# Performance work log

Hardware: AMD Instinct MI355X
Metric: run time of the kernel (lower is better)

## Reference

```python
import jax, jax.numpy as jnp
import numpy as np

B_GRAPHS = 16
N_PER_GRAPH = 128
N_NODES = B_GRAPHS * N_PER_GRAPH  # 2048
HIDDEN = 256
N_HEADS = 8
HEAD_DIM = HIDDEN // N_HEADS
N_LAYERS = 4
K_RPE = 4
N_EDGES = 32768
NUM_NODE_FEATS = 32
NUM_EDGE_TYPES = 16
MAX_DEGREE = 100
MLP_HID = HIDDEN // 2


def _layernorm(x, s, b):
    m = x.mean(-1, keepdims=True)
    v = jnp.var(x, axis=-1, keepdims=True)
    return (x - m) / jnp.sqrt(v + 1e-5) * s + b


def setup_inputs() -> dict:
    key = jax.random.key(0)
    ks = jax.random.split(key, 24)
    s = 0.02
    x_idx = jax.random.randint(ks[0], (N_NODES,), 0, NUM_NODE_FEATS)
    # edges are intra-graph (the torch code drops cross-graph edges)
    src = jax.random.randint(ks[1], (N_EDGES,), 0, N_NODES)
    dst = (src // N_PER_GRAPH) * N_PER_GRAPH + jax.random.randint(ks[2], (N_EDGES,), 0, N_PER_GRAPH)
    edge_index = jnp.stack([src, dst])
    edge_attr = jax.random.randint(ks[3], (N_EDGES,), 0, NUM_EDGE_TYPES)
    batch = jnp.repeat(jnp.arange(B_GRAPHS), N_PER_GRAPH)
    L = N_LAYERS
    return {
        'x_idx': x_idx, 'edge_index': edge_index, 'edge_attr': edge_attr, 'batch': batch,
        'node_emb': jax.random.normal(ks[4], (NUM_NODE_FEATS, HIDDEN)) * s,
        'edge_emb': jax.random.normal(ks[5], (NUM_EDGE_TYPES, N_HEADS)) * s,
        'degree_emb': jax.random.normal(ks[6], (MAX_DEGREE + 1, HIDDEN)) * s,
        'rpe_W1': jax.random.normal(ks[7], (K_RPE + 1, MLP_HID)) * s,
        'rpe_b1': jnp.zeros((MLP_HID,)),
        'rpe_W2': jax.random.normal(ks[8], (MLP_HID, N_HEADS)) * s,
        'rpe_b2': jnp.zeros((N_HEADS,)),
        'Wq': jax.random.normal(ks[9], (L, HIDDEN, HIDDEN)) * s, 'bq': jnp.zeros((L, HIDDEN)),
        'Wk': jax.random.normal(ks[10], (L, HIDDEN, HIDDEN)) * s, 'bk': jnp.zeros((L, HIDDEN)),
        'Wv': jax.random.normal(ks[11], (L, HIDDEN, HIDDEN)) * s, 'bv': jnp.zeros((L, HIDDEN)),
        'Wo': jax.random.normal(ks[12], (L, HIDDEN, HIDDEN)) * s, 'bo': jnp.zeros((L, HIDDEN)),
        'ln1_s': jnp.ones((L, HIDDEN)), 'ln1_b': jnp.zeros((L, HIDDEN)),
        'ln2_s': jnp.ones((L, HIDDEN)), 'ln2_b': jnp.zeros((L, HIDDEN)),
        'ff_W1': jax.random.normal(ks[13], (L, HIDDEN, 2 * HIDDEN)) * s, 'ff_b1': jnp.zeros((L, 2 * HIDDEN)),
        'ff_W2': jax.random.normal(ks[14], (L, 2 * HIDDEN, HIDDEN)) * s, 'ff_b2': jnp.zeros((L, HIDDEN)),
    }


def _forward(x_idx, edge_index, edge_attr, batch,
             node_emb, edge_emb, degree_emb, rpe_W1, rpe_b1, rpe_W2, rpe_b2,
             Wq, bq, Wk, bk, Wv, bv, Wo, bo, ln1_s, ln1_b, ln2_s, ln2_b,
             ff_W1, ff_b1, ff_W2, ff_b2):
    B, n, H, N = B_GRAPHS, N_PER_GRAPH, N_HEADS, N_NODES
    x = node_emb[x_idx]                               # [N, d]
    src, dst = edge_index[0], edge_index[1]
    # degrees from source endpoints (scatter_add in torch)
    deg = jnp.zeros((N,), jnp.int32).at[src].add(1)
    deg_c = jnp.minimum(deg, MAX_DEGREE)

    # ---- RRWP + edge-type attention bias, block-diagonal over graphs ----
    g = batch[src]
    intra = (batch[src] == batch[dst])                # torch code skips cross-graph edges
    u = src % n
    v = dst % n
    intra_f = intra.astype(jnp.float32)
    inv_du = intra_f / jnp.maximum(deg[src], 1).astype(jnp.float32)
    inv_dv = intra_f / jnp.maximum(deg[dst], 1).astype(jnp.float32)
    # random-walk transition matrix per graph [B, n, n]
    T = (jnp.zeros((B, n, n), jnp.float32)
         .at[g, u, v].add(inv_du)
         .at[g, v, u].add(inv_dv))
    # symmetric edge-type bias per graph [B, n, n, H]
    ev = edge_emb[edge_attr] * intra_f[:, None]
    EB = (jnp.zeros((B, n, n, H), jnp.float32)
          .at[g, u, v].add(ev)
          .at[g, v, u].add(ev))
    # walk powers I, T, T^2, ..., T^K -> [B, n, n, K+1]
    I = jnp.broadcast_to(jnp.eye(n, dtype=jnp.float32), (B, n, n))
    powers = [I, T]
    cur = T
    for _ in range(2, K_RPE + 1):
        cur = cur @ T
        powers.append(cur)
    walk = jnp.stack(powers, axis=-1)
    pair = jax.nn.relu(walk @ rpe_W1 + rpe_b1) @ rpe_W2 + rpe_b2   # [B, n, n, H]
    block = (pair + EB).transpose(0, 3, 1, 2)                      # [B, H, n, n]
    ib = jnp.arange(B)
    full = jnp.full((H, B, n, B, n), -jnp.inf, jnp.float32)
    full = full.at[:, ib, :, ib, :].set(block)                     # diag blocks
    attn_bias = full.reshape(H, N, N)

    # ---- transformer stack ----
    deg_vec = degree_emb[deg_c]
    scale = 1.0 / jnp.sqrt(jnp.float32(HEAD_DIM))
    for l in range(N_LAYERS):
        x = x + deg_vec
        Q = (x @ Wq[l] + bq[l]).reshape(N, H, HEAD_DIM)
        K_ = (x @ Wk[l] + bk[l]).reshape(N, H, HEAD_DIM)
        V = (x @ Wv[l] + bv[l]).reshape(N, H, HEAD_DIM)
        scores = jnp.einsum('ihd,jhd->hij', Q, K_) * scale + attn_bias
        aw = jax.nn.softmax(scores, axis=-1)
        out = jnp.einsum('hij,jhd->ihd', aw, V).reshape(N, HIDDEN)
        out = out @ Wo[l] + bo[l]
        x = _layernorm(x + out, ln1_s[l], ln1_b[l])
        ff = jax.nn.relu(x @ ff_W1[l] + ff_b1[l]) @ ff_W2[l] + ff_b2[l]
        x = _layernorm(x + ff, ln2_s[l], ln2_b[l])
    # global add pool
    return jax.ops.segment_sum(x, batch, num_segments=B)


def reference(x_idx, edge_index, edge_attr, batch,
              node_emb, edge_emb, degree_emb, rpe_W1, rpe_b1, rpe_W2, rpe_b2,
              Wq, bq, Wk, bk, Wv, bv, Wo, bo, ln1_s, ln1_b, ln2_s, ln2_b,
              ff_W1, ff_b1, ff_W2, ff_b2):
    return _forward(x_idx, edge_index, edge_attr, batch,
                    node_emb, edge_emb, degree_emb, rpe_W1, rpe_b1, rpe_W2, rpe_b2,
                    Wq, bq, Wk, bk, Wv, bv, Wo, bo, ln1_s, ln1_b, ln2_s, ln2_b,
                    ff_W1, ff_b1, ff_W2, ff_b2)
```

## Files before the change

### kernel.cpp

```cpp
#include <hip/hip_runtime.h>
#include <hip/hip_bf16.h>

#define B_GRAPHS 16
#define NPG 128
#define NN 2048
#define HIDDEN 256
#define N_HEADS 8
#define HEAD_DIM 32
#define N_LAYERS 4
#define N_EDGES 32768
#define MLP_HID 128
#define MAX_DEG 100

typedef __hip_bfloat16 bf16;
typedef unsigned short ushort_t;
typedef __attribute__((ext_vector_type(8))) short short8;
typedef __attribute__((ext_vector_type(4))) float f32x4;

__device__ __forceinline__ float us2f(ushort_t u) {
    return __uint_as_float(((unsigned)u) << 16);
}
__device__ __forceinline__ ushort_t f2us(float f) {
    unsigned u = __float_as_uint(f);
    return (ushort_t)((u + 0x7FFFu + ((u >> 16) & 1u)) >> 16);
}
__device__ __forceinline__ bool is_bf16_mode(const unsigned* probe) {
    return probe[0] != 0x3F800000u;
}
#define MFMA16(a, b, c) __builtin_amdgcn_mfma_f32_16x16x32_bf16(a, b, c, 0, 0, 0)

#define NW 23
__device__ const int c_wsizes[NW] = {
    8192, 128, 25856, 640, 128, 1024, 8,
    262144, 1024, 262144, 1024, 262144, 1024, 262144, 1024,
    1024, 1024, 1024, 1024,
    524288, 2048, 524288, 1024};
#define TOTW 2144392

#define OFF_NODE_EMB 0
#define OFF_EDGE_EMB 8192
#define OFF_DEG_EMB  8320
#define OFF_RPE_W1   34176
#define OFF_RPE_B1   34816
#define OFF_RPE_W2   34944
#define OFF_RPE_B2   35968
#define OFF_BO       1087624
#define OFF_LN1S     1088648
#define OFF_LN1B     1089672
#define OFF_LN2S     1090696
#define OFF_LN2B     1091720
#define OFF_FFB1     1617032
#define OFF_FFB2     2143368

#define WB_QKV 0
#define WB_O   786432
#define WB_F1  1048576
#define WB_F2  1572864
#define WB_TOT 2097152
#define QKVB_TOT 3072

struct SrcPtrs { const void* p[NW]; };

__global__ void convert_kernel(SrcPtrs sp, const unsigned* __restrict__ probe,
                               float* __restrict__ Wc, float* __restrict__ qkvb) {
    int i = blockIdx.x * 256 + threadIdx.x;
    bool isbf = is_bf16_mode(probe);
    auto rd = [&](int seg, int off) -> float {
        return isbf ? us2f(((const ushort_t*)sp.p[seg])[off])
                    : ((const float*)sp.p[seg])[off];
    };
    if (i < TOTW) {
        int seg = 0, off = i;
        while (seg < NW - 1 && off >= c_wsizes[seg]) { off -= c_wsizes[seg]; seg++; }
        Wc[i] = rd(seg, off);
    } else if (i < TOTW + QKVB_TOT) {
        int j = i - TOTW;
        int l = j / 768, n = j % 768, which = n >> 8, nn = n & 255;
        int seg = (which == 0) ? 8 : (which == 1) ? 10 : 12;
        qkvb[j] = rd(seg, l * 256 + nn);
    }
}

__global__ __launch_bounds__(256) void transpose_pack(SrcPtrs sp,
                                                      const unsigned* __restrict__ probe,
                                                      ushort_t* __restrict__ WB) {
    __shared__ float tile[32][33];
    int b = blockIdx.x;
    bool isbf = is_bf16_mode(probe);
    int seg, soff, srcN, k0, n0, dK;
    size_t doff;
    if (b < 768) {
        int mat = b >> 6, t = b & 63;
        int l = mat / 3, which = mat % 3;
        seg = 7 + which * 2;
        soff = l * 65536; srcN = 256;
        k0 = (t >> 3) * 32; n0 = (t & 7) * 32;
        doff = (size_t)l * 196608 + (size_t)which * 65536; dK = 256;
    } else if (b < 1024) {
        int u = b - 768, l = u >> 6, t = u & 63;
        seg = 13; soff = l * 65536; srcN = 256;
        k0 = (t >> 3) * 32; n0 = (t & 7) * 32;
        doff = WB_O + (size_t)l * 65536; dK = 256;
    } else if (b < 1536) {
        int u = b - 1024, l = u >> 7, t = u & 127;
        seg = 19; soff = l * 131072; srcN = 512;
        k0 = (t >> 4) * 32; n0 = (t & 15) * 32;
        doff = WB_F1 + (size_t)l * 131072; dK = 256;
    } else {
        int u = b - 1536, l = u >> 7, t = u & 127;
        seg = 21; soff = l * 131072; srcN = 256;
        k0 = (t >> 3) * 32; n0 = (t & 7) * 32;
        doff = WB_F2 + (size_t)l * 131072; dK = 512;
    }
    int xcol = threadIdx.x & 31, y8 = threadIdx.x >> 5;
    const void* srcp = sp.p[seg];
#pragma unroll
    for (int rr = 0; rr < 4; rr++) {
        int row = y8 * 4 + rr;
        int off = soff + (k0 + row) * srcN + n0 + xcol;
        tile[row][xcol] = isbf ? us2f(((const ushort_t*)srcp)[off])
                               : ((const float*)srcp)[off];
    }
    __syncthreads();
#pragma unroll
    for (int rr = 0; rr < 4; rr++) {
        int nrow = y8 * 4 + rr;
        WB[doff + (size_t)(n0 + nrow) * dK + k0 + xcol] = f2us(tile[xcol][nrow]);
    }
}

__global__ void zero_kernel(f32x4* __restrict__ p) {
    f32x4 z;
    z[0] = 0.f; z[1] = 0.f; z[2] = 0.f; z[3] = 0.f;
    p[blockIdx.x * 256 + threadIdx.x] = z;
}

__global__ void deg_kernel(const int* __restrict__ src, int* __restrict__ deg) {
    int e = blockIdx.x * blockDim.x + threadIdx.x;
    if (e < N_EDGES) atomicAdd(&deg[src[e]], 1);
}

__global__ void gather_xadd(const int* __restrict__ xidx, const int* __restrict__ deg,
                            const float* __restrict__ emb, const float* __restrict__ demb,
                            float* __restrict__ x, ushort_t* __restrict__ xb) {
    int i = blockIdx.x * blockDim.x + threadIdx.x;
    int node = i >> 8, c = i & 255;
    float v = emb[xidx[node] * HIDDEN + c] + demb[min(deg[node], MAX_DEG) * HIDDEN + c];
    x[i] = v;
    xb[i] = f2us(v);
}

__global__ void scatter_kernel(const int* __restrict__ ei, const int* __restrict__ eattr,
                               const int* __restrict__ batch, const int* __restrict__ deg,
                               const float* __restrict__ edge_emb,
                               float* __restrict__ T, float* __restrict__ bias) {
    int idx = blockIdx.x * blockDim.x + threadIdx.x;
    int e = idx >> 3, h = idx & 7;
    int s = ei[e], d = ei[N_EDGES + e];
    if (batch[s] != batch[d]) return;
    int g = batch[s];
    int u = s & (NPG - 1), v = d & (NPG - 1);
    if (h == 0) {
        atomicAdd(&T[(g * NPG + u) * NPG + v], 1.0f / (float)max(deg[s], 1));
        atomicAdd(&T[(g * NPG + v) * NPG + u], 1.0f / (float)max(deg[d], 1));
    }
    float ev = edge_emb[eattr[e] * N_HEADS + h];
    atomicAdd(&bias[(((size_t)(g * N_HEADS + h) * NPG + u) * NPG + v)], ev);
    atomicAdd(&bias[(((size_t)(g * N_HEADS + h) * NPG + v) * NPG + u)], ev);
}

__global__ void matmul128(const float* __restrict__ A, const float* __restrict__ B,
                          float* __restrict__ C) {
    int g = blockIdx.x / NPG;
    int row = blockIdx.x % NPG;
    int col = threadIdx.x;
    const float* Ag = A + (size_t)g * NPG * NPG;
    const float* Bg = B + (size_t)g * NPG * NPG;
    __shared__ float arow[NPG];
    arow[col] = Ag[row * NPG + col];
    __syncthreads();
    float acc = 0.f;
#pragma unroll 8
    for (int k = 0; k < NPG; k++) acc += arow[k] * Bg[k * NPG + col];
    C[((size_t)g * NPG + row) * NPG + col] = acc;
}

__global__ void matmul128_dual(const float* __restrict__ T2, const float* __restrict__ T,
                               float* __restrict__ T3, float* __restrict__ T4) {
    int half = blockIdx.x >> 11;
    int bid = blockIdx.x & 2047;
    int g = bid / NPG, row = bid % NPG, col = threadIdx.x;
    const float* Ag = T2 + (size_t)g * NPG * NPG;
    const float* Bg = (half ? T2 : T) + (size_t)g * NPG * NPG;
    float* Cg = (half ? T4 : T3) + (size_t)g * NPG * NPG;
    __shared__ float arow[NPG];
    arow[col] = Ag[row * NPG + col];
    __syncthreads();
    float acc = 0.f;
#pragma unroll 8
    for (int k = 0; k < NPG; k++) acc += arow[k] * Bg[k * NPG + col];
    Cg[row * NPG + col] = acc;
}

__global__ __launch_bounds__(256) void rpe_kernel(
    const float* __restrict__ T, const float* __restrict__ T2,
    const float* __restrict__ T3, const float* __restrict__ T4,
    const float* __restrict__ W1, const float* __restrict__ b1,
    const float* __restrict__ W2, const float* __restrict__ b2,
    float* __restrict__ bias) {
    __shared__ float sW1[5][MLP_HID];
    __shared__ float sb1[MLP_HID];
    __shared__ float sW2[MLP_HID][N_HEADS];
    int t = threadIdx.x;
    for (int i = t; i < 5 * MLP_HID; i += 256) sW1[i / MLP_HID][i % MLP_HID] = W1[i];
    for (int i = t; i < MLP_HID; i += 256) sb1[i] = b1[i];
    for (int i = t; i < MLP_HID * N_HEADS; i += 256) sW2[i / N_HEADS][i % N_HEADS] = W2[i];
    __syncthreads();
    int p = blockIdx.x * 256 + t;
    int g = p / (NPG * NPG);
    int rem = p % (NPG * NPG);
    int i = rem / NPG, j = rem % NPG;
    float f0 = (i == j) ? 1.f : 0.f;
    float f1 = T[p], f2 = T2[p], f3 = T3[p], f4 = T4[p];
    float acc[N_HEADS];
#pragma unroll
    for (int h = 0; h < N_HEADS; h++) acc[h] = b2[h];
#pragma unroll 4
    for (int m = 0; m < MLP_HID; m++) {
        float hv = sb1[m] + f0 * sW1[0][m] + f1 * sW1[1][m] + f2 * sW1[2][m] +
                   f3 * sW1[3][m] + f4 * sW1[4][m];
        hv = fmaxf(hv, 0.f);
#pragma unroll
        for (int h = 0; h < N_HEADS; h++) acc[h] += hv * sW2[m][h];
    }
#pragma unroll
    for (int h = 0; h < N_HEADS; h++)
        bias[(((size_t)(g * N_HEADS + h) * NPG + i) * NPG + j)] += acc[h];
}

__global__ __launch_bounds__(256, 1) void qkv_attn(
    const ushort_t* __restrict__ x_bf, const ushort_t* __restrict__ WT,
    const float* __restrict__ qb, const float* __restrict__ bias,
    ushort_t* __restrict__ ao) {
    int bid = blockIdx.x;
    int g = bid >> 4, h = (bid >> 1) & 7, half = bid & 1;
    int wave = threadIdx.x >> 6, lane = threadIdx.x & 63;
    int lr = lane & 15, lq = lane >> 4;

    __shared__ ushort_t Qs[64][40];
    __shared__ ushort_t Ks[NPG][40];
    __shared__ ushort_t VT[32][136];
    __shared__ ushort_t P[4][16][136];

    const ushort_t* xg = x_bf + (size_t)g * NPG * HIDDEN;
    int qrow = half * 64 + wave * 16;
    int kvrow = wave * 32;

    short8 Aq[8], Akv[2][8], Bq[2][8], Bk[2][8], Bv[2][8];
#pragma unroll
    for (int kk = 0; kk < 8; kk++) {
        Aq[kk] = *(const short8*)(xg + (size_t)(qrow + lr) * 256 + kk * 32 + lq * 8);
#pragma unroll
        for (int i = 0; i < 2; i++)
            Akv[i][kk] = *(const short8*)(xg + (size_t)(kvrow + i * 16 + lr) * 256 +
                                          kk * 32 + lq * 8);
#pragma unroll
        for (int j = 0; j < 2; j++) {
            int n = h * 32 + j * 16 + lr;
            Bq[j][kk] = *(const short8*)(WT + (size_t)n * 256 + kk * 32 + lq * 8);
            Bk[j][kk] = *(const short8*)(WT + (size_t)(n + 256) * 256 + kk * 32 + lq * 8);
            Bv[j][kk] = *(const short8*)(WT + (size_t)(n + 512) * 256 + kk * 32 + lq * 8);
        }
    }
    float bqv[2], bkv[2], bvv[2];
#pragma unroll
    for (int j = 0; j < 2; j++) {
        int c = h * 32 + j * 16 + lr;
        bqv[j] = qb[c]; bkv[j] = qb[256 + c]; bvv[j] = qb[512 + c];
    }

    f32x4 qa[2]{}, ka[2][2]{}, va[2][2]{};
#pragma unroll
    for (int kk = 0; kk < 8; kk++)
#pragma unroll
        for (int j = 0; j < 2; j++) {
            qa[j] = MFMA16(Aq[kk], Bq[j][kk], qa[j]);
#pragma unroll
            for (int i = 0; i < 2; i++) {
                ka[i][j] = MFMA16(Akv[i][kk], Bk[j][kk], ka[i][j]);
                va[i][j] = MFMA16(Akv[i][kk], Bv[j][kk], va[i][j]);
            }
        }

    const float* bg = bias + (size_t)(g * N_HEADS + h) * NPG * NPG;
    float bgv[8][4];
#pragma unroll
    for (int r = 0; r < 4; r++) {
        int i = half * 64 + wave * 16 + lq * 4 + r;
#pragma unroll
        for (int jt = 0; jt < 8; jt++)
            bgv[jt][r] = bg[(size_t)i * NPG + jt * 16 + lr];
    }

#pragma unroll
    for (int j = 0; j < 2; j++) {
        int c = j * 16 + lr;
#pragma unroll
        for (int r = 0; r < 4; r++) {
            Qs[wave * 16 + lq * 4 + r][c] = f2us(qa[j][r] + bqv[j]);
#pragma unroll
            for (int i = 0; i < 2; i++) {
                int row = kvrow + i * 16 + lq * 4 + r;
                Ks[row][c] = f2us(ka[i][j][r] + bkv[j]);
                VT[c][row] = f2us(va[i][j][r] + bvv[j]);
            }
        }
    }
    __syncthreads();

    short8 qf = *(const short8*)(&Qs[wave * 16 + lr][lq * 8]);
    f32x4 S[8];
    f32x4 zero;
    zero[0] = 0.f; zero[1] = 0.f; zero[2] = 0.f; zero[3] = 0.f;
#pragma unroll
    for (int jt = 0; jt < 8; jt++) {
        short8 kf = *(const short8*)(&Ks[jt * 16 + lr][lq * 8]);
        S[jt] = MFMA16(qf, kf, zero);
    }

    const float scale = 0.17677669529663687f;
    float lrow[4];
#pragma unroll
    for (int r = 0; r < 4; r++) {
        float mx = -1e30f;
#pragma unroll
        for (int jt = 0; jt < 8; jt++) {
            float s = S[jt][r] * scale + bgv[jt][r];
            S[jt][r] = s;
            mx = fmaxf(mx, s);
        }
#pragma unroll
        for (int m = 1; m < 16; m <<= 1) mx = fmaxf(mx, __shfl_xor(mx, m));
        float sum = 0.f;
#pragma unroll
        for (int jt = 0; jt < 8; jt++) {
            float e = __expf(S[jt][r] - mx);
            S[jt][r] = e;
            sum += e;
        }
#pragma unroll
        for (int m = 1; m < 16; m <<= 1) sum += __shfl_xor(sum, m);
        lrow[r] = sum;
    }

#pragma unroll
    for (int jt = 0; jt < 8; jt++)
#pragma unroll
        for (int r = 0; r < 4; r++)
            P[wave][lq * 4 + r][jt * 16 + lr] = f2us(S[jt][r]);

    f32x4 O[2]{};
#pragma unroll
    for (int k0 = 0; k0 < NPG; k0 += 32) {
        short8 pa = *(const short8*)(&P[wave][lr][k0 + lq * 8]);
#pragma unroll
        for (int dt = 0; dt < 2; dt++) {
            short8 vb = *(const short8*)(&VT[dt * 16 + lr][k0 + lq * 8]);
            O[dt] = MFMA16(pa, vb, O[dt]);
        }
    }
#pragma unroll
    for (int r = 0; r < 4; r++) {
        float inv = 1.f / lrow[r];
        int row = g * NPG + half * 64 + wave * 16 + lq * 4 + r;
#pragma unroll
        for (int dt = 0; dt < 2; dt++)
            ao[(size_t)row * HIDDEN + h * 32 + dt * 16 + lr] = f2us(O[dt][r] * inv);
    }
}

__global__ __launch_bounds__(256, 1) void fused_mlp(
    const ushort_t* __restrict__ ao, const ushort_t* __restrict__ WoT,
    const float* __restrict__ bo, const float* __restrict__ ln1s,
    const float* __restrict__ ln1b,
    const ushort_t* __restrict__ F1T, const ushort_t* __restrict__ F2T,
    const float* __restrict__ fb1, const float* __restrict__ fb2,
    const float* __restrict__ ln2s, const float* __restrict__ ln2b,
    const float* __restrict__ xin, const int* __restrict__ deg,
    const float* __restrict__ demb, int add_deg,
    float* __restrict__ xout, ushort_t* __restrict__ xb) {
    int m0 = blockIdx.x * 8;
    int wave = threadIdx.x >> 6, lane = threadIdx.x & 63;
    int lr = lane & 15, lq = lane >> 4;
    int ar = m0 + (lr & 7);

    __shared__ ushort_t xs_bf[8][264];
    __shared__ float xs_f[8][256];
    __shared__ ushort_t ffh[8][520];
    __shared__ float ws[4][16], qs[4][16];

    short8 Ao[8], Bo[4][8];
#pragma unroll
    for (int kk = 0; kk < 8; kk++) {
        Ao[kk] = *(const short8*)(ao + (size_t)ar * 256 + kk * 32 + lq * 8);
#pragma unroll
        for (int jt = 0; jt < 4; jt++) {
            int n = wave * 64 + jt * 16 + lr;
            Bo[jt][kk] = *(const short8*)(WoT + (size_t)n * 256 + kk * 32 + lq * 8);
        }
    }
    float bo_v[4], l1s[4], l1b[4], fb2v[4], l2s[4], l2b[4], xres[4][4], fb1v[8];
#pragma unroll
    for (int jt = 0; jt < 4; jt++) {
        int col = wave * 64 + jt * 16 + lr;
        bo_v[jt] = bo[col]; l1s[jt] = ln1s[col]; l1b[jt] = ln1b[col];
        fb2v[jt] = fb2[col]; l2s[jt] = ln2s[col]; l2b[jt] = ln2b[col];
#pragma unroll
        for (int r = 0; r < 4; r++) {
            int row = m0 + ((lq * 4 + r) & 7);
            xres[jt][r] = xin[(size_t)row * 256 + col];
        }
    }
#pragma unroll
    for (int jt = 0; jt < 8; jt++) fb1v[jt] = fb1[wave * 128 + jt * 16 + lr];
    int dg4[4];
    if (add_deg) {
#pragma unroll
        for (int r = 0; r < 4; r++)
            dg4[r] = min(deg[m0 + ((lq * 4 + r) & 7)], MAX_DEG);
    }

    f32x4 acc[4]{};
#pragma unroll
    for (int kk = 0; kk < 8; kk++)
#pragma unroll
        for (int jt = 0; jt < 4; jt++)
            acc[jt] = MFMA16(Ao[kk], Bo[jt][kk], acc[jt]);

    short8 B1[8][8];
#pragma unroll
    for (int kk = 0; kk < 8; kk++)
#pragma unroll
        for (int jt = 0; jt < 8; jt++) {
            int n = wave * 128 + jt * 16 + lr;
            B1[jt][kk] = *(const short8*)(F1T + (size_t)n * 256 + kk * 32 + lq * 8);
        }

    float val[4][4], meanst[4];
#pragma unroll
    for (int r = 0; r < 4; r++) {
        float s = 0.f;
#pragma unroll
        for (int jt = 0; jt < 4; jt++) {
            float v = acc[jt][r] + bo_v[jt] + xres[jt][r];
            val[jt][r] = v;
            s += v;
        }
#pragma unroll
        for (int m = 1; m < 16; m <<= 1) s += __shfl_xor(s, m);
        if (lr == 0) ws[wave][lq * 4 + r] = s;
    }
    __syncthreads();
#pragma unroll
    for (int r = 0; r < 4; r++) {
        int rr = lq * 4 + r;
        float mean = (ws[0][rr] + ws[1][rr] + ws[2][rr] + ws[3][rr]) * (1.f / 256.f);
        meanst[r] = mean;
        float q = 0.f;
#pragma unroll
        for (int jt = 0; jt < 4; jt++) {
            float d = val[jt][r] - mean;
            q += d * d;
        }
#pragma unroll
        for (int m = 1; m < 16; m <<= 1) q += __shfl_xor(q, m);
        if (lr == 0) qs[wave][rr] = q;
    }
    __syncthreads();
#pragma unroll
    for (int r = 0; r < 4; r++) {
        int rr = lq * 4 + r;
        float var = (qs[0][rr] + qs[1][rr] + qs[2][rr] + qs[3][rr]) * (1.f / 256.f);
        float rstd = rsqrtf(var + 1e-5f);
        if (rr < 8) {
#pragma unroll
            for (int jt = 0; jt < 4; jt++) {
                int col = wave * 64 + jt * 16 + lr;
                float y = (val[jt][r] - meanst[r]) * rstd * l1s[jt] + l1b[jt];
                xs_f[rr][col] = y;
                xs_bf[rr][col] = f2us(y);
            }
        }
    }
    __syncthreads();

    f32x4 acc1[8]{};
#pragma unroll
    for (int kk = 0; kk < 8; kk++) {
        short8 a = *(const short8*)(&xs_bf[lr & 7][kk * 32 + lq * 8]);
#pragma unroll
        for (int jt = 0; jt < 8; jt++)
            acc1[jt] = MFMA16(a, B1[jt][kk], acc1[jt]);
    }

    short8 B2[4][16];
#pragma unroll
    for (int kk = 0; kk < 16; kk++)
#pragma unroll
        for (int jt = 0; jt < 4; jt++) {
            int n = wave * 64 + jt * 16 + lr;
            B2[jt][kk] = *(const short8*)(F2T + (size_t)n * 512 + kk * 32 + lq * 8);
        }

#pragma unroll
    for (int jt = 0; jt < 8; jt++) {
        int n = wave * 128 + jt * 16 + lr;
#pragma unroll
        for (int r = 0; r < 4; r++) {
            int rr = lq * 4 + r;
            if (rr < 8) ffh[rr][n] = f2us(fmaxf(acc1[jt][r] + fb1v[jt], 0.f));
        }
    }
    __syncthreads();

    f32x4 acc2[4]{};
#pragma unroll
    for (int kk = 0; kk < 16; kk++) {
        short8 a = *(const short8*)(&ffh[lr & 7][kk * 32 + lq * 8]);
#pragma unroll
        for (int jt = 0; jt < 4; jt++)
            acc2[jt] = MFMA16(a, B2[jt][kk], acc2[jt]);
    }

#pragma unroll
    for (int r = 0; r < 4; r++) {
        int rr = lq * 4 + r;
        float s = 0.f;
#pragma unroll
        for (int jt = 0; jt < 4; jt++) {
            int col = wave * 64 + jt * 16 + lr;
            float v = acc2[jt][r] + fb2v[jt] + xs_f[rr & 7][col];
            val[jt][r] = v;
            s += v;
        }
#pragma unroll
        for (int m = 1; m < 16; m <<= 1) s += __shfl_xor(s, m);
        if (lr == 0) ws[wave][rr] = s;
    }
    __syncthreads();
#pragma unroll
    for (int r = 0; r < 4; r++) {
        int rr = lq * 4 + r;
        float mean = (ws[0][rr] + ws[1][rr] + ws[2][rr] + ws[3][rr]) * (1.f / 256.f);
        meanst[r] = mean;
        float q = 0.f;
#pragma unroll
        for (int jt = 0; jt < 4; jt++) {
            float d = val[jt][r] - mean;
            q += d * d;
        }
#pragma unroll
        for (int m = 1; m < 16; m <<= 1) q += __shfl_xor(q, m);
        if (lr == 0) qs[wave][rr] = q;
    }
    __syncthreads();
#pragma unroll
    for (int r = 0; r < 4; r++) {
        int rr = lq * 4 + r;
        float var = (qs[0][rr] + qs[1][rr] + qs[2][rr] + qs[3][rr]) * (1.f / 256.f);
        float rstd = rsqrtf(var + 1e-5f);
        if (rr < 8) {
            int row = m0 + rr;
#pragma unroll
            for (int jt = 0; jt < 4; jt++) {
                int col = wave * 64 + jt * 16 + lr;
                float y = (val[jt][r] - meanst[r]) * rstd * l2s[jt] + l2b[jt];
                if (add_deg) y += demb[dg4[r] * 256 + col];
                xout[(size_t)row * 256 + col] = y;
                xb[(size_t)row * 256 + col] = f2us(y);
            }
        }
    }
}

__global__ void pool_kernel(const float* __restrict__ x, void* __restrict__ out,
                            const unsigned* __restrict__ probe) {
    int b = blockIdx.x;
    int c = threadIdx.x;
    float acc = 0.f;
#pragma unroll 4
    for (int i = 0; i < NPG; i++) acc += x[(size_t)(b * NPG + i) * HIDDEN + c];
    if (is_bf16_mode(probe))
        ((bf16*)out)[b * HIDDEN + c] = __float2bfloat16(acc);
    else
        ((float*)out)[b * HIDDEN + c] = acc;
}

extern "C" void kernel_launch(void* const* d_in, const int* in_sizes, int n_in,
                              void* d_out, int out_size, void* d_ws, size_t ws_size,
                              hipStream_t stream) {
    const int* x_idx      = (const int*)d_in[0];
    const int* edge_index = (const int*)d_in[1];
    const int* edge_attr  = (const int*)d_in[2];
    const int* batch      = (const int*)d_in[3];
    const unsigned* probe = (const unsigned*)d_in[19];

    char* base = (char*)d_ws;
    float* Wc    = (float*)base;       base += (size_t)TOTW * 4;
    float* x     = (float*)base;       base += (size_t)NN * HIDDEN * 4;
    float* T     = (float*)base;       base += 262144 * 4;
    float* bias  = (float*)base;       base += (size_t)2097152 * 4;
    int*   deg   = (int*)base;         base += 2048 * 4;
    float* T2    = (float*)base;       base += 262144 * 4;
    float* T3    = (float*)base;       base += 262144 * 4;
    float* T4    = (float*)base;       base += 262144 * 4;
    float* qkvb  = (float*)base;       base += QKVB_TOT * 4;
    ushort_t* WB    = (ushort_t*)base; base += (size_t)WB_TOT * 2;
    ushort_t* x_bf  = (ushort_t*)base; base += (size_t)NN * HIDDEN * 2;
    ushort_t* ao_bf = (ushort_t*)base; base += (size_t)NN * HIDDEN * 2;

    SrcPtrs sp;
    for (int i = 0; i < NW; i++) sp.p[i] = d_in[4 + i];

    zero_kernel<<<2306, 256, 0, stream>>>((f32x4*)T);
    convert_kernel<<<(TOTW + QKVB_TOT + 255) / 256, 256, 0, stream>>>(sp, probe, Wc, qkvb);
    transpose_pack<<<2048, 256, 0, stream>>>(sp, probe, WB);
    deg_kernel<<<N_EDGES / 256, 256, 0, stream>>>(edge_index, deg);
    gather_xadd<<<NN, 256, 0, stream>>>(x_idx, deg, Wc + OFF_NODE_EMB, Wc + OFF_DEG_EMB,
                                        x, x_bf);
    scatter_kernel<<<N_EDGES * 8 / 256, 256, 0, stream>>>(edge_index, edge_attr, batch, deg,
                                                          Wc + OFF_EDGE_EMB, T, bias);
    matmul128<<<B_GRAPHS * NPG, NPG, 0, stream>>>(T, T, T2);
    matmul128_dual<<<2 * B_GRAPHS * NPG, NPG, 0, stream>>>(T2, T, T3, T4);
    rpe_kernel<<<(B_GRAPHS * NPG * NPG) / 256, 256, 0, stream>>>(
        T, T2, T3, T4, Wc + OFF_RPE_W1, Wc + OFF_RPE_B1, Wc + OFF_RPE_W2, Wc + OFF_RPE_B2,
        bias);

    for (int l = 0; l < N_LAYERS; l++) {
        qkv_attn<<<2 * B_GRAPHS * N_HEADS, 256, 0, stream>>>(
            x_bf, WB + WB_QKV + (size_t)l * 196608, qkvb + l * 768, bias, ao_bf);
        fused_mlp<<<NN / 8, 256, 0, stream>>>(
            ao_bf, WB + WB_O + (size_t)l * 65536, Wc + OFF_BO + l * 256,
            Wc + OFF_LN1S + l * 256, Wc + OFF_LN1B + l * 256,
            WB + WB_F1 + (size_t)l * 131072, WB + WB_F2 + (size_t)l * 131072,
            Wc + OFF_FFB1 + l * 512, Wc + OFF_FFB2 + l * 256,
            Wc + OFF_LN2S + l * 256, Wc + OFF_LN2B + l * 256, x,
            deg, Wc + OFF_DEG_EMB, (l < N_LAYERS - 1) ? 1 : 0, x, x_bf);
    }
    pool_kernel<<<B_GRAPHS, 256, 0, stream>>>(x, d_out, probe);
}
```

Measured before the change: 385.0 us.

## Shrink fused_mlp rows per block to 4 and chunk weight loads for occupancy

The fused output-projection/FFN/layernorm kernel now handles 4 rows per block instead of 8, doubling the grid to 512 blocks, and asks for 2 blocks per CU via launch bounds. Weight fragments for F1 and F2 are loaded in K-chunks rather than all at once, and the fp32 LN1 output is kept in registers instead of shared memory. This cuts register and LDS pressure so more waves can hide global-load latency. The cost is twice the total weight traffic from L2, since each block still streams the full weight matrices while MFMA 16-row tiles are now only a quarter used.

```diff
diff --git a/kernel.cpp b/kernel.cpp
--- a/kernel.cpp
+++ b/kernel.cpp
@@ -379,7 +379,7 @@
     }
 }
 
-__global__ __launch_bounds__(256, 1) void fused_mlp(
+__global__ __launch_bounds__(256, 2) void fused_mlp(
     const ushort_t* __restrict__ ao, const ushort_t* __restrict__ WoT,
     const float* __restrict__ bo, const float* __restrict__ ln1s,
     const float* __restrict__ ln1b,
@@ -389,192 +389,190 @@
     const float* __restrict__ xin, const int* __restrict__ deg,
     const float* __restrict__ demb, int add_deg,
     float* __restrict__ xout, ushort_t* __restrict__ xb) {
-    int m0 = blockIdx.x * 8;
-    int wave = threadIdx.x >> 6, lane = threadIdx.x & 63;
+    int m0 = blockIdx.x * 4;
+    int w = threadIdx.x >> 6, lane = threadIdx.x & 63;
     int lr = lane & 15, lq = lane >> 4;
-    int ar = m0 + (lr & 7);
-
-    __shared__ ushort_t xs_bf[8][264];
-    __shared__ float xs_f[8][256];
-    __shared__ ushort_t ffh[8][520];
-    __shared__ float ws[4][16], qs[4][16];
-
-    short8 Ao[8], Bo[4][8];
-#pragma unroll
-    for (int kk = 0; kk < 8; kk++) {
-        Ao[kk] = *(const short8*)(ao + (size_t)ar * 256 + kk * 32 + lq * 8);
-#pragma unroll
-        for (int jt = 0; jt < 4; jt++) {
-            int n = wave * 64 + jt * 16 + lr;
-            Bo[jt][kk] = *(const short8*)(WoT + (size_t)n * 256 + kk * 32 + lq * 8);
-        }
-    }
+    int ar = m0 + (lr & 3);
+
+    __shared__ ushort_t xs_bf[4][264];
+    __shared__ ushort_t ffh[4][520];
+    __shared__ float part[4][4], qpart[4][4];
+
     float bo_v[4], l1s[4], l1b[4], fb2v[4], l2s[4], l2b[4], xres[4][4], fb1v[8];
 #pragma unroll
     for (int jt = 0; jt < 4; jt++) {
-        int col = wave * 64 + jt * 16 + lr;
+        int col = w * 64 + jt * 16 + lr;
         bo_v[jt] = bo[col]; l1s[jt] = ln1s[col]; l1b[jt] = ln1b[col];
         fb2v[jt] = fb2[col]; l2s[jt] = ln2s[col]; l2b[jt] = ln2b[col];
 #pragma unroll
-        for (int r = 0; r < 4; r++) {
-            int row = m0 + ((lq * 4 + r) & 7);
-            xres[jt][r] = xin[(size_t)row * 256 + col];
-        }
-    }
-#pragma unroll
-    for (int jt = 0; jt < 8; jt++) fb1v[jt] = fb1[wave * 128 + jt * 16 + lr];
+        for (int r = 0; r < 4; r++)
+            xres[jt][r] = xin[(size_t)(m0 + r) * 256 + col];
+    }
+#pragma unroll
+    for (int jt = 0; jt < 8; jt++) fb1v[jt] = fb1[w * 128 + jt * 16 + lr];
     int dg4[4];
     if (add_deg) {
 #pragma unroll
-        for (int r = 0; r < 4; r++)
-            dg4[r] = min(deg[m0 + ((lq * 4 + r) & 7)], MAX_DEG);
+        for (int r = 0; r < 4; r++) dg4[r] = min(deg[m0 + r], MAX_DEG);
     }
 
     f32x4 acc[4]{};
-#pragma unroll
-    for (int kk = 0; kk < 8; kk++)
-#pragma unroll
-        for (int jt = 0; jt < 4; jt++)
-            acc[jt] = MFMA16(Ao[kk], Bo[jt][kk], acc[jt]);
-
-    short8 B1[8][8];
-#pragma unroll
-    for (int kk = 0; kk < 8; kk++)
-#pragma unroll
-        for (int jt = 0; jt < 8; jt++) {
-            int n = wave * 128 + jt * 16 + lr;
-            B1[jt][kk] = *(const short8*)(F1T + (size_t)n * 256 + kk * 32 + lq * 8);
-        }
-
-    float val[4][4], meanst[4];
+    {
+        short8 Ao[8], Bo[4][8];
+#pragma unroll
+        for (int kk = 0; kk < 8; kk++) {
+            Ao[kk] = *(const short8*)(ao + (size_t)ar * 256 + kk * 32 + lq * 8);
+#pragma unroll
+            for (int jt = 0; jt < 4; jt++) {
+                int n = w * 64 + jt * 16 + lr;
+                Bo[jt][kk] = *(const short8*)(WoT + (size_t)n * 256 + kk * 32 + lq * 8);
+            }
+        }
+#pragma unroll
+        for (int kk = 0; kk < 8; kk++)
+#pragma unroll
+            for (int jt = 0; jt < 4; jt++)
+                acc[jt] = MFMA16(Ao[kk], Bo[jt][kk], acc[jt]);
+    }
+
+    float valLN[4][4], meanst[4];
 #pragma unroll
     for (int r = 0; r < 4; r++) {
         float s = 0.f;
 #pragma unroll
         for (int jt = 0; jt < 4; jt++) {
             float v = acc[jt][r] + bo_v[jt] + xres[jt][r];
-            val[jt][r] = v;
+            valLN[jt][r] = v;
             s += v;
         }
 #pragma unroll
         for (int m = 1; m < 16; m <<= 1) s += __shfl_xor(s, m);
-        if (lr == 0) ws[wave][lq * 4 + r] = s;
-    }
-    __syncthreads();
-#pragma unroll
-    for (int r = 0; r < 4; r++) {
-        int rr = lq * 4 + r;
-        float mean = (ws[0][rr] + ws[1][rr] + ws[2][rr] + ws[3][rr]) * (1.f / 256.f);
+        if (lane == 0) part[w][r] = s;
+    }
+    __syncthreads();
+#pragma unroll
+    for (int r = 0; r < 4; r++) {
+        float mean = (part[0][r] + part[1][r] + part[2][r] + part[3][r]) * (1.f / 256.f);
         meanst[r] = mean;
         float q = 0.f;
 #pragma unroll
         for (int jt = 0; jt < 4; jt++) {
-            float d = val[jt][r] - mean;
+            float d = valLN[jt][r] - mean;
             q += d * d;
         }
 #pragma unroll
         for (int m = 1; m < 16; m <<= 1) q += __shfl_xor(q, m);
-        if (lr == 0) qs[wave][rr] = q;
-    }
-    __syncthreads();
-#pragma unroll
-    for (int r = 0; r < 4; r++) {
-        int rr = lq * 4 + r;
-        float var = (qs[0][rr] + qs[1][rr] + qs[2][rr] + qs[3][rr]) * (1.f / 256.f);
+        if (lane == 0) qpart[w][r] = q;
+    }
+    __syncthreads();
+#pragma unroll
+    for (int r = 0; r < 4; r++) {
+        float var = (qpart[0][r] + qpart[1][r] + qpart[2][r] + qpart[3][r]) * (1.f / 256.f);
         float rstd = rsqrtf(var + 1e-5f);
-        if (rr < 8) {
+#pragma unroll
+        for (int jt = 0; jt < 4; jt++) {
+            int col = w * 64 + jt * 16 + lr;
+            float y = (valLN[jt][r] - meanst[r]) * rstd * l1s[jt] + l1b[jt];
+            valLN[jt][r] = y;
+            xs_bf[r][col] = f2us(y);
+        }
+    }
+    __syncthreads();
+
+    f32x4 acc1[8]{};
+#pragma unroll
+    for (int kc = 0; kc < 2; kc++) {
+        short8 B1[8][4];
+#pragma unroll
+        for (int k4 = 0; k4 < 4; k4++) {
+            int kk = kc * 4 + k4;
+#pragma unroll
+            for (int jt = 0; jt < 8; jt++) {
+                int n = w * 128 + jt * 16 + lr;
+                B1[jt][k4] = *(const short8*)(F1T + (size_t)n * 256 + kk * 32 + lq * 8);
+            }
+        }
+#pragma unroll
+        for (int k4 = 0; k4 < 4; k4++) {
+            int kk = kc * 4 + k4;
+            short8 a = *(const short8*)(&xs_bf[lr & 3][kk * 32 + lq * 8]);
+#pragma unroll
+            for (int jt = 0; jt < 8; jt++)
+                acc1[jt] = MFMA16(a, B1[jt][k4], acc1[jt]);
+        }
+    }
+#pragma unroll
+    for (int jt = 0; jt < 8; jt++) {
+        int n = w * 128 + jt * 16 + lr;
+#pragma unroll
+        for (int r = 0; r < 4; r++)
+            ffh[r][n] = f2us(fmaxf(acc1[jt][r] + fb1v[jt], 0.f));
+    }
+    __syncthreads();
+
+    f32x4 acc2[4]{};
+#pragma unroll
+    for (int kc = 0; kc < 2; kc++) {
+        short8 B2[4][8];
+#pragma unroll
+        for (int k8 = 0; k8 < 8; k8++) {
+            int kk = kc * 8 + k8;
 #pragma unroll
             for (int jt = 0; jt < 4; jt++) {
-                int col = wave * 64 + jt * 16 + lr;
-                float y = (val[jt][r] - meanst[r]) * rstd * l1s[jt] + l1b[jt];
-                xs_f[rr][col] = y;
-                xs_bf[rr][col] = f2us(y);
+                int n = w * 64 + jt * 16 + lr;
+                B2[jt][k8] = *(const short8*)(F2T + (size_t)n * 512 + kk * 32 + lq * 8);
             }
         }
-    }
-    __syncthreads();
-
-    f32x4 acc1[8]{};
-#pragma unroll
-    for (int kk = 0; kk < 8; kk++) {
-        short8 a = *(const short8*)(&xs_bf[lr & 7][kk * 32 + lq * 8]);
-#pragma unroll
-        for (int jt = 0; jt < 8; jt++)
-            acc1[jt] = MFMA16(a, B1[jt][kk], acc1[jt]);
-    }
-
-    short8 B2[4][16];
-#pragma unroll
-    for (int kk = 0; kk < 16; kk++)
+#pragma unroll
+        for (int k8 = 0; k8 < 8; k8++) {
+            int kk = kc * 8 + k8;
+            short8 a = *(const short8*)(&ffh[lr & 3][kk * 32 + lq * 8]);
+#pragma unroll
+            for (int jt = 0; jt < 4; jt++)
+                acc2[jt] = MFMA16(a, B2[jt][k8], acc2[jt]);
+        }
+    }
+
+    float val2[4][4];
+#pragma unroll
+    for (int r = 0; r < 4; r++) {
+        float s = 0.f;
 #pragma unroll
         for (int jt = 0; jt < 4; jt++) {
-            int n = wave * 64 + jt * 16 + lr;
-            B2[jt][kk] = *(const short8*)(F2T + (size_t)n * 512 + kk * 32 + lq * 8);
-        }
-
-#pragma unroll
-    for (int jt = 0; jt < 8; jt++) {
-        int n = wave * 128 + jt * 16 + lr;
-#pragma unroll
-        for (int r = 0; r < 4; r++) {
-            int rr = lq * 4 + r;
-            if (rr < 8) ffh[rr][n] = f2us(fmaxf(acc1[jt][r] + fb1v[jt], 0.f));
-        }
-    }
-    __syncthreads();
-
-    f32x4 acc2[4]{};
-#pragma unroll
-    for (int kk = 0; kk < 16; kk++) {
-        short8 a = *(const short8*)(&ffh[lr & 7][kk * 32 + lq * 8]);
-#pragma unroll
-        for (int jt = 0; jt < 4; jt++)
-            acc2[jt] = MFMA16(a, B2[jt][kk], acc2[jt]);
-    }
-
-#pragma unroll
-    for (int r = 0; r < 4; r++) {
-        int rr = lq * 4 + r;
-        float s = 0.f;
-#pragma unroll
-        for (int jt = 0; jt < 4; jt++) {
-            int col = wave * 64 + jt * 16 + lr;
-            float v = acc2[jt][r] + fb2v[jt] + xs_f[rr & 7][col];
-            val[jt][r] = v;
+            float v = acc2[jt][r] + fb2v[jt] + valLN[jt][r];
+            val2[jt][r] = v;
             s += v;
         }
 #pragma unroll
         for (int m = 1; m < 16; m <<= 1) s += __shfl_xor(s, m);
-        if (lr == 0) ws[wave][rr] = s;
-    }
-    __syncthreads();
-#pragma unroll
-    for (int r = 0; r < 4; r++) {
-        int rr = lq * 4 + r;
-        float mean = (ws[0][rr] + ws[1][rr] + ws[2][rr] + ws[3][rr]) * (1.f / 256.f);
+        if (lane == 0) part[w][r] = s;
+    }
+    __syncthreads();
+#pragma unroll
+    for (int r = 0; r < 4; r++) {
+        float mean = (part[0][r] + part[1][r] + part[2][r] + part[3][r]) * (1.f / 256.f);
         meanst[r] = mean;
         float q = 0.f;
 #pragma unroll
         for (int jt = 0; jt < 4; jt++) {
-            float d = val[jt][r] - mean;
+            float d = val2[jt][r] - mean;
             q += d * d;
         }
 #pragma unroll
         for (int m = 1; m < 16; m <<= 1) q += __shfl_xor(q, m);
-        if (lr == 0) qs[wave][rr] = q;
-    }
-    __syncthreads();
-#pragma unroll
-    for (int r = 0; r < 4; r++) {
-        int rr = lq * 4 + r;
-        float var = (qs[0][rr] + qs[1][rr] + qs[2][rr] + qs[3][rr]) * (1.f / 256.f);
+        if (lane == 0) qpart[w][r] = q;
+    }
+    __syncthreads();
+#pragma unroll
+    for (int r = 0; r < 4; r++) {
+        float var = (qpart[0][r] + qpart[1][r] + qpart[2][r] + qpart[3][r]) * (1.f / 256.f);
         float rstd = rsqrtf(var + 1e-5f);
-        if (rr < 8) {
-            int row = m0 + rr;
+        int row = m0 + r;
+        if (lq == 0) {
 #pragma unroll
             for (int jt = 0; jt < 4; jt++) {
-                int col = wave * 64 + jt * 16 + lr;
-                float y = (val[jt][r] - meanst[r]) * rstd * l2s[jt] + l2b[jt];
+                int col = w * 64 + jt * 16 + lr;
+                float y = (val2[jt][r] - meanst[r]) * rstd * l2s[jt] + l2b[jt];
                 if (add_deg) y += demb[dg4[r] * 256 + col];
                 xout[(size_t)row * 256 + col] = y;
                 xb[(size_t)row * 256 + col] = f2us(y);
@@ -639,7 +637,7 @@
     for (int l = 0; l < N_LAYERS; l++) {
         qkv_attn<<<2 * B_GRAPHS * N_HEADS, 256, 0, stream>>>(
             x_bf, WB + WB_QKV + (size_t)l * 196608, qkvb + l * 768, bias, ao_bf);
-        fused_mlp<<<NN / 8, 256, 0, stream>>>(
+        fused_mlp<<<NN / 4, 256, 0, stream>>>(
             ao_bf, WB + WB_O + (size_t)l * 65536, Wc + OFF_BO + l * 256,
             Wc + OFF_LN1S + l * 256, Wc + OFF_LN1B + l * 256,
             WB + WB_F1 + (size_t)l * 131072, WB + WB_F2 + (size_t)l * 131072,
```

New measurement: 442.5 us. 14.9% more time.

## Stream MLP weights through double-buffered LDS with async global-to-LDS loads

Applied to the files above, without the earlier changes.

The fused output-projection and feed-forward kernel used to load the Wo, FF1 and FF2 weights straight into large register arrays. It now streams them in 64KB chunks into a double-buffered, XOR-swizzled LDS area using global_load_lds. Each chunk overlaps with MFMA compute on the previous chunk through manual vmcnt waits and barriers. The fp32 LayerNorm residual is also kept in registers instead of an LDS array. This cuts register pressure and exposed load latency, at the cost of 128KB of LDS per block and more barriers.

```diff
diff --git a/kernel.cpp b/kernel.cpp
--- a/kernel.cpp
+++ b/kernel.cpp
@@ -28,6 +28,17 @@
     return probe[0] != 0x3F800000u;
 }
 #define MFMA16(a, b, c) __builtin_amdgcn_mfma_f32_16x16x32_bf16(a, b, c, 0, 0, 0)
+
+__device__ __forceinline__ void gload_lds16(const void* g, void* l) {
+    __builtin_amdgcn_global_load_lds(
+        (const __attribute__((address_space(1))) unsigned int*)g,
+        (__attribute__((address_space(3))) unsigned int*)l, 16, 0, 0);
+}
+#define SBAR __builtin_amdgcn_s_barrier()
+#define WAITPIPE asm volatile("s_waitcnt vmcnt(16) lgkmcnt(0)" ::: "memory")
+#define WAITLAST asm volatile("s_waitcnt vmcnt(0) lgkmcnt(0)" ::: "memory")
+#define LBAR do { asm volatile("s_waitcnt lgkmcnt(0)" ::: "memory"); SBAR; \
+                  asm volatile("" ::: "memory"); } while (0)
 
 #define NW 23
 __device__ const int c_wsizes[NW] = {
@@ -394,22 +405,46 @@
     int lr = lane & 15, lq = lane >> 4;
     int ar = m0 + (lr & 7);
 
+    __shared__ ushort_t Wbuf[2][32768];
     __shared__ ushort_t xs_bf[8][264];
-    __shared__ float xs_f[8][256];
     __shared__ ushort_t ffh[8][520];
     __shared__ float ws[4][16], qs[4][16];
 
-    short8 Ao[8], Bo[4][8];
-#pragma unroll
-    for (int kk = 0; kk < 8; kk++) {
-        Ao[kk] = *(const short8*)(ao + (size_t)ar * 256 + kk * 32 + lq * 8);
-#pragma unroll
-        for (int jt = 0; jt < 4; jt++) {
-            int n = wave * 64 + jt * 16 + lr;
-            Bo[jt][kk] = *(const short8*)(WoT + (size_t)n * 256 + kk * 32 + lq * 8);
-        }
-    }
-    float bo_v[4], l1s[4], l1b[4], fb2v[4], l2s[4], l2b[4], xres[4][4], fb1v[8];
+    auto stageO = [&](int h, int b) {
+        const char* gW = (const char*)WoT;
+        char* lb = (char*)&Wbuf[b][0] + wave * 16384;
+#pragma unroll
+        for (int it = 0; it < 16; it++) {
+            int j = wave * 16384 + it * 1024 + lane * 16;
+            int n = j >> 8, off = j & 255;
+            gload_lds16(gW + n * 512 + h * 256 + (off ^ ((n & 7) << 4)), lb + it * 1024);
+        }
+        __builtin_amdgcn_sched_barrier(0);
+    };
+    auto stageF1 = [&](int q, int b) {
+        const char* gW = (const char*)F1T;
+        char* lb = (char*)&Wbuf[b][0] + wave * 16384;
+#pragma unroll
+        for (int it = 0; it < 16; it++) {
+            int j = wave * 16384 + it * 1024 + lane * 16;
+            int n = j >> 9, off = j & 511;
+            gload_lds16(gW + (q * 128 + n) * 512 + (off ^ ((n & 7) << 4)), lb + it * 1024);
+        }
+        __builtin_amdgcn_sched_barrier(0);
+    };
+    auto stageF2 = [&](int q, int b) {
+        const char* gW = (const char*)F2T;
+        char* lb = (char*)&Wbuf[b][0] + wave * 16384;
+#pragma unroll
+        for (int it = 0; it < 16; it++) {
+            int j = wave * 16384 + it * 1024 + lane * 16;
+            int n = j >> 8, off = j & 255;
+            gload_lds16(gW + n * 1024 + q * 256 + (off ^ ((n & 7) << 4)), lb + it * 1024);
+        }
+        __builtin_amdgcn_sched_barrier(0);
+    };
+
+    float bo_v[4], l1s[4], l1b[4], fb2v[4], l2s[4], l2b[4], xres[4][4], fb1q[4][2];
 #pragma unroll
     for (int jt = 0; jt < 4; jt++) {
         int col = wave * 64 + jt * 16 + lr;
@@ -422,45 +457,59 @@
         }
     }
 #pragma unroll
-    for (int jt = 0; jt < 8; jt++) fb1v[jt] = fb1[wave * 128 + jt * 16 + lr];
+    for (int q = 0; q < 4; q++)
+#pragma unroll
+        for (int t = 0; t < 2; t++)
+            fb1q[q][t] = fb1[q * 128 + wave * 32 + t * 16 + lr];
     int dg4[4];
     if (add_deg) {
 #pragma unroll
         for (int r = 0; r < 4; r++)
             dg4[r] = min(deg[m0 + ((lq * 4 + r) & 7)], MAX_DEG);
     }
+    short8 Af[8];
+#pragma unroll
+    for (int t = 0; t < 8; t++)
+        Af[t] = *(const short8*)(ao + (size_t)ar * 256 + t * 32 + lq * 8);
+
+    stageO(0, 0);
+    stageO(1, 1);
 
     f32x4 acc[4]{};
 #pragma unroll
-    for (int kk = 0; kk < 8; kk++)
-#pragma unroll
-        for (int jt = 0; jt < 4; jt++)
-            acc[jt] = MFMA16(Ao[kk], Bo[jt][kk], acc[jt]);
-
-    short8 B1[8][8];
-#pragma unroll
-    for (int kk = 0; kk < 8; kk++)
-#pragma unroll
-        for (int jt = 0; jt < 8; jt++) {
-            int n = wave * 128 + jt * 16 + lr;
-            B1[jt][kk] = *(const short8*)(F1T + (size_t)n * 256 + kk * 32 + lq * 8);
-        }
-
-    float val[4][4], meanst[4];
+    for (int h = 0; h < 2; h++) {
+        WAITPIPE; SBAR; asm volatile("" ::: "memory");
+#pragma unroll
+        for (int kk = 0; kk < 4; kk++) {
+            short8 a = Af[h * 4 + kk];
+#pragma unroll
+            for (int jt = 0; jt < 4; jt++) {
+                int n = wave * 64 + jt * 16 + lr;
+                int bo_ = n * 256 + ((kk * 64 + lq * 16) ^ ((n & 7) << 4));
+                short8 bf = *(const short8*)((const char*)&Wbuf[h][0] + bo_);
+                acc[jt] = MFMA16(a, bf, acc[jt]);
+            }
+        }
+        LBAR;
+        if (h == 0) stageF1(0, 0);
+        else        stageF1(1, 1);
+    }
+
+    float valLN[4][4], meanst[4];
 #pragma unroll
     for (int r = 0; r < 4; r++) {
         float s = 0.f;
 #pragma unroll
         for (int jt = 0; jt < 4; jt++) {
             float v = acc[jt][r] + bo_v[jt] + xres[jt][r];
-            val[jt][r] = v;
+            valLN[jt][r] = v;
             s += v;
         }
 #pragma unroll
         for (int m = 1; m < 16; m <<= 1) s += __shfl_xor(s, m);
         if (lr == 0) ws[wave][lq * 4 + r] = s;
     }
-    __syncthreads();
+    LBAR;
 #pragma unroll
     for (int r = 0; r < 4; r++) {
         int rr = lq * 4 + r;
@@ -469,78 +518,86 @@
         float q = 0.f;
 #pragma unroll
         for (int jt = 0; jt < 4; jt++) {
-            float d = val[jt][r] - mean;
+            float d = valLN[jt][r] - mean;
             q += d * d;
         }
 #pragma unroll
         for (int m = 1; m < 16; m <<= 1) q += __shfl_xor(q, m);
         if (lr == 0) qs[wave][rr] = q;
     }
-    __syncthreads();
+    LBAR;
 #pragma unroll
     for (int r = 0; r < 4; r++) {
         int rr = lq * 4 + r;
         float var = (qs[0][rr] + qs[1][rr] + qs[2][rr] + qs[3][rr]) * (1.f / 256.f);
         float rstd = rsqrtf(var + 1e-5f);
-        if (rr < 8) {
+#pragma unroll
+        for (int jt = 0; jt < 4; jt++) {
+            int col = wave * 64 + jt * 16 + lr;
+            float y = (valLN[jt][r] - meanst[r]) * rstd * l1s[jt] + l1b[jt];
+            valLN[jt][r] = y;
+            if (rr < 8) xs_bf[rr][col] = f2us(y);
+        }
+    }
+
+#pragma unroll
+    for (int q = 0; q < 4; q++) {
+        WAITPIPE; SBAR; asm volatile("" ::: "memory");
+        f32x4 a1[2]{};
+#pragma unroll
+        for (int kk = 0; kk < 8; kk++) {
+            short8 a = *(const short8*)(&xs_bf[lr & 7][kk * 32 + lq * 8]);
+#pragma unroll
+            for (int t = 0; t < 2; t++) {
+                int n = wave * 32 + t * 16 + lr;
+                int bo_ = n * 512 + ((kk * 64 + lq * 16) ^ ((n & 7) << 4));
+                short8 bf = *(const short8*)((const char*)&Wbuf[q & 1][0] + bo_);
+                a1[t] = MFMA16(a, bf, a1[t]);
+            }
+        }
+#pragma unroll
+        for (int t = 0; t < 2; t++) {
+            int col = q * 128 + wave * 32 + t * 16 + lr;
+#pragma unroll
+            for (int r = 0; r < 4; r++) {
+                int rr = lq * 4 + r;
+                if (rr < 8) ffh[rr][col] = f2us(fmaxf(a1[t][r] + fb1q[q][t], 0.f));
+            }
+        }
+        LBAR;
+        if (q < 2) stageF1(q + 2, q & 1);
+        else       stageF2(q - 2, q & 1);
+    }
+
+    f32x4 acc2[4]{};
+#pragma unroll
+    for (int q = 0; q < 4; q++) {
+        if (q == 3) { WAITLAST; } else { WAITPIPE; }
+        SBAR; asm volatile("" ::: "memory");
+#pragma unroll
+        for (int kk = 0; kk < 4; kk++) {
+            short8 a = *(const short8*)(&ffh[lr & 7][q * 128 + kk * 32 + lq * 8]);
 #pragma unroll
             for (int jt = 0; jt < 4; jt++) {
-                int col = wave * 64 + jt * 16 + lr;
-                float y = (val[jt][r] - meanst[r]) * rstd * l1s[jt] + l1b[jt];
-                xs_f[rr][col] = y;
-                xs_bf[rr][col] = f2us(y);
+                int n = wave * 64 + jt * 16 + lr;
+                int bo_ = n * 256 + ((kk * 64 + lq * 16) ^ ((n & 7) << 4));
+                short8 bf = *(const short8*)((const char*)&Wbuf[q & 1][0] + bo_);
+                acc2[jt] = MFMA16(a, bf, acc2[jt]);
             }
         }
-    }
-    __syncthreads();
-
-    f32x4 acc1[8]{};
-#pragma unroll
-    for (int kk = 0; kk < 8; kk++) {
-        short8 a = *(const short8*)(&xs_bf[lr & 7][kk * 32 + lq * 8]);
-#pragma unroll
-        for (int jt = 0; jt < 8; jt++)
-            acc1[jt] = MFMA16(a, B1[jt][kk], acc1[jt]);
-    }
-
-    short8 B2[4][16];
-#pragma unroll
-    for (int kk = 0; kk < 16; kk++)
-#pragma unroll
-        for (int jt = 0; jt < 4; jt++) {
-            int n = wave * 64 + jt * 16 + lr;
-            B2[jt][kk] = *(const short8*)(F2T + (size_t)n * 512 + kk * 32 + lq * 8);
-        }
-
-#pragma unroll
-    for (int jt = 0; jt < 8; jt++) {
-        int n = wave * 128 + jt * 16 + lr;
-#pragma unroll
-        for (int r = 0; r < 4; r++) {
-            int rr = lq * 4 + r;
-            if (rr < 8) ffh[rr][n] = f2us(fmaxf(acc1[jt][r] + fb1v[jt], 0.f));
-        }
-    }
-    __syncthreads();
-
-    f32x4 acc2[4]{};
-#pragma unroll
-    for (int kk = 0; kk < 16; kk++) {
-        short8 a = *(const short8*)(&ffh[lr & 7][kk * 32 + lq * 8]);
-#pragma unroll
-        for (int jt = 0; jt < 4; jt++)
-            acc2[jt] = MFMA16(a, B2[jt][kk], acc2[jt]);
-    }
-
+        LBAR;
+        if (q < 2) stageF2(q + 2, q & 1);
+    }
+
+    float val2[4][4];
 #pragma unroll
     for (int r = 0; r < 4; r++) {
         int rr = lq * 4 + r;
         float s = 0.f;
 #pragma unroll
         for (int jt = 0; jt < 4; jt++) {
-            int col = wave * 64 + jt * 16 + lr;
-            float v = acc2[jt][r] + fb2v[jt] + xs_f[rr & 7][col];
-            val[jt][r] = v;
+            float v = acc2[jt][r] + fb2v[jt] + valLN[jt][r];
+            val2[jt][r] = v;
             s += v;
         }
 #pragma unroll
@@ -556,7 +613,7 @@
         float q = 0.f;
 #pragma unroll
         for (int jt = 0; jt < 4; jt++) {
-            float d = val[jt][r] - mean;
+            float d = val2[jt][r] - mean;
             q += d * d;
         }
 #pragma unroll
@@ -574,7 +631,7 @@
 #pragma unroll
             for (int jt = 0; jt < 4; jt++) {
                 int col = wave * 64 + jt * 16 + lr;
-                float y = (val[jt][r] - meanst[r]) * rstd * l2s[jt] + l2b[jt];
+                float y = (val2[jt][r] - meanst[r]) * rstd * l2s[jt] + l2b[jt];
                 if (add_deg) y += demb[dg4[r] * 256 + col];
                 xout[(size_t)row * 256 + col] = y;
                 xb[(size_t)row * 256 + col] = f2us(y);
```

After: 356.8 us. -7.3%, faster.
